# Performance work log

Hardware: AMD Instinct MI355X
Metric: run time of the kernel (lower is better)

## Reference

```python
import jax, jax.numpy as jnp
import numpy as np

RETURN_INDEX = 0  # return_index init kwarg
D_MODEL = 64
NUM_FEATURES = 362


def setup_inputs() -> dict:
    key = jax.random.key(0)
    k1, k2, k3, k4, k5 = jax.random.split(key, 5)
    B, S, N, F, D = 4, 128, 512, NUM_FEATURES, D_MODEL
    x = jax.random.normal(k1, (B, S, N, F), dtype=jnp.float32)
    s = 1.0 / np.sqrt(F)  # torch nn.Linear default init bound
    Wg_w = jax.random.uniform(k2, (D, F), minval=-s, maxval=s, dtype=jnp.float32)
    Wg_b = jax.random.uniform(k3, (D,), minval=-s, maxval=s, dtype=jnp.float32)
    Wh_w = jax.random.uniform(k4, (D, F), minval=-s, maxval=s, dtype=jnp.float32)
    Wh_b = jax.random.uniform(k5, (D,), minval=-s, maxval=s, dtype=jnp.float32)
    return {"x": x, "Wg_w": Wg_w, "Wg_b": Wg_b, "Wh_w": Wh_w, "Wh_b": Wh_b}


def reference(x, Wg_w, Wg_b, Wh_w, Wh_b):
    # x: [B, S, N, F]. Haar dwt -> idwt(cA,None)/idwt(None,cD) collapses to:
    #   rec_l[2k] = rec_l[2k+1] = (x[2k]+x[2k+1])/2
    #   rec_h[2k] = -rec_h[2k+1] = (x[2k]-x[2k+1])/2
    B, S, N, F = x.shape
    r = x[:, :, :, RETURN_INDEX]                      # [B, S, N]
    rp = r.reshape(B, S // 2, 2, N)                   # pair adjacent time steps
    avg = (rp[:, :, 0] + rp[:, :, 1]) * 0.5           # [B, S//2, N]
    diff = (rp[:, :, 0] - rp[:, :, 1]) * 0.5          # [B, S//2, N]
    X_l = jnp.stack([avg, avg], axis=2).reshape(B, S, N)
    X_h = jnp.stack([diff, -diff], axis=2).reshape(B, S, N)
    X_l_full = x.at[:, :, :, RETURN_INDEX].set(X_l)
    X_h_full = x.at[:, :, :, RETURN_INDEX].set(X_h)
    X_l_proj = jnp.einsum('bsnf,df->bsnd', X_l_full, Wg_w) + Wg_b
    X_h_proj = jnp.einsum('bsnf,df->bsnd', X_h_full, Wh_w) + Wh_b
    return (X_l_proj, X_h_proj)
```

## Files before the change

kernel.cpp:

```cpp
#include <hip/hip_runtime.h>
#include <hip/hip_bf16.h>
#include <stdint.h>

#define M_ROWS (4*128*512)
#define FDIM 362
#define TROWS 16
#define ROWB 1448
#define TILEB (TROWS*ROWB)
#define CPW 362
#define GRID 1024
#define TPB 16
#define OUT_HALF 16777216

typedef __attribute__((ext_vector_type(8))) short bf16x8;
typedef __attribute__((ext_vector_type(4))) float f32x4;

template<int N> struct Ic { static constexpr int value = N; };

__device__ __forceinline__ bf16x8 pack8(float2 a, float2 b, float2 c, float2 d) {
  union { __hip_bfloat162 h[4]; bf16x8 v; } t;
  t.h[0] = __float22bfloat162_rn(a);
  t.h[1] = __float22bfloat162_rn(b);
  t.h[2] = __float22bfloat162_rn(c);
  t.h[3] = __float22bfloat162_rn(d);
  return t.v;
}
__device__ __forceinline__ float2 ld2(const float* p) { return *(const float2*)p; }

__global__ __launch_bounds__(256, 2) void dfl_kernel(
    const float* __restrict__ x,
    const float* __restrict__ Wg,
    const float* __restrict__ Wgb,
    const float* __restrict__ Wh,
    const float* __restrict__ Whb,
    float* __restrict__ out)
{
  __shared__ __attribute__((aligned(16))) unsigned char Ab[3][TILEB];
  __shared__ __attribute__((aligned(16))) unsigned char tb[4*2048];

  const int tid  = threadIdx.x;
  const int lane = tid & 63;
  const int wv   = tid >> 6;
  const int q    = lane >> 4;
  const int l15  = lane & 15;
  const bool is_h = wv >= 2;
  const int colb  = (wv & 1) * 32;
  const float* Wsel  = is_h ? Wh  : Wg;
  const float* Wbsel = is_h ? Whb : Wgb;

  bf16x8 bw[2][12];
  float biasf[2], w0f[2];
#pragma unroll
  for (int f = 0; f < 2; ++f) {
    const int dloc = colb + f*16 + l15;
    const float* wrow = Wsel + (size_t)dloc * FDIM;
    biasf[f] = Wbsel[dloc];
    w0f[f]   = wrow[0];
#pragma unroll
    for (int k = 0; k < 12; ++k) {
      float2 t0 = make_float2(0.f,0.f), t1 = t0, t2 = t0, t3 = t0;
      if (k < 11) {
        const float* p = wrow + k*32 + q*8;
        t0 = ld2(p); t1 = ld2(p+2); t2 = ld2(p+4); t3 = ld2(p+6);
      } else if (q == 0) {
        t0 = ld2(wrow+352); t1 = ld2(wrow+354); t2 = ld2(wrow+356); t3 = ld2(wrow+358);
      } else if (q == 1) {
        t0 = ld2(wrow+360);
      }
      bw[f][k] = pack8(t0, t1, t2, t3);
    }
  }

  auto stage = [&](int tile, int p) {
    const unsigned char* src = (const unsigned char*)(x + (size_t)tile * TROWS * FDIM);
    unsigned char* dst = &Ab[p][0];
#pragma unroll
    for (int j = 0; j < 6; ++j) {
      const int cbase = wv*CPW + j*64;
      if (lane < CPW - j*64) {
        __builtin_amdgcn_global_load_lds(
            (const __attribute__((address_space(1))) unsigned int*)(src + (size_t)(cbase + lane)*16),
            (__attribute__((address_space(3))) unsigned int*)(dst + cbase*16),
            16, 0, 0);
      }
    }
  };

  unsigned char* wb = tb + wv*2048;
  float* outp = out + (is_h ? OUT_HALF : 0) + colb;

  auto round = [&](int i, auto sflag, auto wc) {
    const int p  = i % 3;
    const int m0 = ((int)blockIdx.x + i*GRID) * TROWS;

    const float rp = x[(size_t)((m0 ^ 512) + l15) * FDIM];
    __builtin_amdgcn_sched_barrier(0);
    if constexpr (decltype(sflag)::value)
      stage((int)blockIdx.x + (i+2)*GRID, (i+2) % 3);
    __builtin_amdgcn_sched_barrier(0);

    const unsigned char* AbP = &Ab[p][0];
    const unsigned char* ap  = AbP + l15*ROWB + q*32;
    f32x4 acc0 = {biasf[0],biasf[0],biasf[0],biasf[0]};
    f32x4 acc1 = {biasf[1],biasf[1],biasf[1],biasf[1]};
#pragma unroll
    for (int k = 0; k < 11; ++k) {
      const unsigned char* pk = ap + k*128;
      bf16x8 av = pack8(*(const float2*)pk, *(const float2*)(pk+8),
                        *(const float2*)(pk+16), *(const float2*)(pk+24));
      acc0 = __builtin_amdgcn_mfma_f32_16x16x32_bf16(av, bw[0][k], acc0, 0,0,0);
      acc1 = __builtin_amdgcn_mfma_f32_16x16x32_bf16(av, bw[1][k], acc1, 0,0,0);
    }
    {
      const unsigned char* pk = ap + 11*128;
      float2 z2 = make_float2(0.f,0.f), f0 = z2, f1 = z2, f2 = z2, f3 = z2;
      if (q == 0) {
        f0 = *(const float2*)pk;      f1 = *(const float2*)(pk+8);
        f2 = *(const float2*)(pk+16); f3 = *(const float2*)(pk+24);
      } else if (q == 1) {
        f0 = *(const float2*)pk;
      }
      bf16x8 av = pack8(f0, f1, f2, f3);
      acc0 = __builtin_amdgcn_mfma_f32_16x16x32_bf16(av, bw[0][11], acc0, 0,0,0);
      acc1 = __builtin_amdgcn_mfma_f32_16x16x32_bf16(av, bw[1][11], acc1, 0,0,0);
    }

    const float rs = *(const float*)(AbP + l15*ROWB);
    const float cval = is_h ? -(rs + rp)*0.5f : (rp - rs)*0.5f;

#pragma unroll
    for (int jj = 0; jj < 4; ++jj) {
      const float cc = __shfl(cval, q*4 + jj, 64);
      const int rl = q*4 + jj;
#pragma unroll
      for (int fn = 0; fn < 2; ++fn) {
        const float v = (fn ? acc1[jj] : acc0[jj]) + cc * w0f[fn];
        const int col = fn*16 + l15;
        const int boff = rl*128 + ((((col>>2) ^ (rl&7))) << 4) + ((col&3) << 2);
        *(float*)(wb + boff) = v;
      }
    }
#pragma unroll
    for (int s = 0; s < 2; ++s) {
      const int rr = s*8 + (lane >> 3);
      const int cs = lane & 7;
      f32x4 vv = *(const f32x4*)(wb + rr*128 + (((cs ^ (rr&7))) << 4));
      *(f32x4*)(outp + (size_t)(m0 + rr)*64 + cs*4) = vv;
    }

    __builtin_amdgcn_sched_barrier(0);
    if constexpr (decltype(wc)::value >= 0) {
      asm volatile("s_waitcnt vmcnt(%0)" :: "i"(decltype(wc)::value) : "memory");
      __builtin_amdgcn_s_barrier();
    }
    __builtin_amdgcn_sched_barrier(0);
  };

  __builtin_amdgcn_sched_barrier(0);
  asm volatile("s_waitcnt vmcnt(0)" ::: "memory");
  stage((int)blockIdx.x, 0);
  stage((int)blockIdx.x + GRID, 1);
  __builtin_amdgcn_sched_barrier(0);
  asm volatile("s_waitcnt vmcnt(6)" ::: "memory");
  __builtin_amdgcn_s_barrier();
  __builtin_amdgcn_sched_barrier(0);

  round(0, Ic<1>{}, Ic<9>{});
  for (int i = 1; i <= 13; ++i) round(i, Ic<1>{}, Ic<11>{});
  round(14, Ic<0>{}, Ic<5>{});
  round(15, Ic<0>{}, Ic<-1>{});
}

extern "C" void kernel_launch(void* const* d_in, const int* in_sizes, int n_in,
                              void* d_out, int out_size, void* d_ws, size_t ws_size,
                              hipStream_t stream) {
  (void)in_sizes; (void)n_in; (void)d_ws; (void)ws_size; (void)out_size;
  const float* x   = (const float*)d_in[0];
  const float* Wg  = (const float*)d_in[1];
  const float* Wgb = (const float*)d_in[2];
  const float* Wh  = (const float*)d_in[3];
  const float* Whb = (const float*)d_in[4];
  float* out = (float*)d_out;
  dfl_kernel<<<GRID, 256, 0, stream>>>(x, Wg, Wgb, Wh, Whb, out);
}
```

Baseline: 117.2 us.

## Switch to double-buffered LDS staging with three blocks per CU

Replaces the hand-scheduled triple-buffered pipeline (fixed 16 rounds, explicit vmcnt waits) with a double-buffered grid-stride loop using __syncthreads. It shrinks the LDS footprint (two tile buffers, a halved transpose buffer written in two halves) and raises launch bounds to 3 blocks per CU with a 768-block grid. The aim is more resident waves to hide memory latency. The trade-off is a shallower prefetch and coarser full waits at each barrier. With 2048 tiles over 768 blocks, work is uneven across blocks.

```diff
diff --git a/kernel.cpp b/kernel.cpp
--- a/kernel.cpp
+++ b/kernel.cpp
@@ -8,14 +8,14 @@
 #define ROWB 1448
 #define TILEB (TROWS*ROWB)
 #define CPW 362
-#define GRID 1024
-#define TPB 16
+#define NTILES (M_ROWS/TROWS)
+#define GRID 768
 #define OUT_HALF 16777216
 
 typedef __attribute__((ext_vector_type(8))) short bf16x8;
 typedef __attribute__((ext_vector_type(4))) float f32x4;
 
-template<int N> struct Ic { static constexpr int value = N; };
+__device__ __forceinline__ float2 ld2(const float* p) { return *(const float2*)p; }
 
 __device__ __forceinline__ bf16x8 pack8(float2 a, float2 b, float2 c, float2 d) {
   union { __hip_bfloat162 h[4]; bf16x8 v; } t;
@@ -25,9 +25,8 @@
   t.h[3] = __float22bfloat162_rn(d);
   return t.v;
 }
-__device__ __forceinline__ float2 ld2(const float* p) { return *(const float2*)p; }
 
-__global__ __launch_bounds__(256, 2) void dfl_kernel(
+__global__ __launch_bounds__(256, 3) void dfl_kernel(
     const float* __restrict__ x,
     const float* __restrict__ Wg,
     const float* __restrict__ Wgb,
@@ -35,8 +34,8 @@
     const float* __restrict__ Whb,
     float* __restrict__ out)
 {
-  __shared__ __attribute__((aligned(16))) unsigned char Ab[3][TILEB];
-  __shared__ __attribute__((aligned(16))) unsigned char tb[4*2048];
+  __shared__ __attribute__((aligned(16))) unsigned char Ab[2][TILEB];
+  __shared__ __attribute__((aligned(16))) unsigned char tb[4*1024];
 
   const int tid  = threadIdx.x;
   const int lane = tid & 63;
@@ -86,21 +85,24 @@
     }
   };
 
-  unsigned char* wb = tb + wv*2048;
+  unsigned char* wb = tb + wv*1024;
   float* outp = out + (is_h ? OUT_HALF : 0) + colb;
 
-  auto round = [&](int i, auto sflag, auto wc) {
-    const int p  = i % 3;
-    const int m0 = ((int)blockIdx.x + i*GRID) * TROWS;
+  int t = (int)blockIdx.x;
+  stage(t, 0);
+  __syncthreads();
+
+  for (int i = 0; t < NTILES; t += GRID, ++i) {
+    const int p  = i & 1;
+    const int m0 = t * TROWS;
+    const int tn = t + GRID;
+    if (tn < NTILES) stage(tn, p ^ 1);
 
     const float rp = x[(size_t)((m0 ^ 512) + l15) * FDIM];
-    __builtin_amdgcn_sched_barrier(0);
-    if constexpr (decltype(sflag)::value)
-      stage((int)blockIdx.x + (i+2)*GRID, (i+2) % 3);
-    __builtin_amdgcn_sched_barrier(0);
 
     const unsigned char* AbP = &Ab[p][0];
     const unsigned char* ap  = AbP + l15*ROWB + q*32;
+
     f32x4 acc0 = {biasf[0],biasf[0],biasf[0],biasf[0]};
     f32x4 acc1 = {biasf[1],biasf[1],biasf[1],biasf[1]};
 #pragma unroll
@@ -129,46 +131,30 @@
     const float cval = is_h ? -(rs + rp)*0.5f : (rp - rs)*0.5f;
 
 #pragma unroll
-    for (int jj = 0; jj < 4; ++jj) {
-      const float cc = __shfl(cval, q*4 + jj, 64);
-      const int rl = q*4 + jj;
+    for (int half = 0; half < 2; ++half) {
 #pragma unroll
-      for (int fn = 0; fn < 2; ++fn) {
-        const float v = (fn ? acc1[jj] : acc0[jj]) + cc * w0f[fn];
-        const int col = fn*16 + l15;
-        const int boff = rl*128 + ((((col>>2) ^ (rl&7))) << 4) + ((col&3) << 2);
-        *(float*)(wb + boff) = v;
+      for (int jj = 0; jj < 4; ++jj) {
+        const int rl = q*4 + jj;
+        const float cc = __shfl(cval, rl, 64);
+        if ((rl >> 3) == half) {
+          const int r7 = rl & 7;
+#pragma unroll
+          for (int fn = 0; fn < 2; ++fn) {
+            const float v = (fn ? acc1[jj] : acc0[jj]) + cc * w0f[fn];
+            const int col = fn*16 + l15;
+            const int boff = r7*128 + ((((col>>2) ^ r7)) << 4) + ((col&3) << 2);
+            *(float*)(wb + boff) = v;
+          }
+        }
       }
-    }
-#pragma unroll
-    for (int s = 0; s < 2; ++s) {
-      const int rr = s*8 + (lane >> 3);
+      const int rr = half*8 + (lane >> 3);
       const int cs = lane & 7;
-      f32x4 vv = *(const f32x4*)(wb + rr*128 + (((cs ^ (rr&7))) << 4));
+      f32x4 vv = *(const f32x4*)(wb + (rr&7)*128 + (((cs ^ (rr&7))) << 4));
       *(f32x4*)(outp + (size_t)(m0 + rr)*64 + cs*4) = vv;
     }
 
-    __builtin_amdgcn_sched_barrier(0);
-    if constexpr (decltype(wc)::value >= 0) {
-      asm volatile("s_waitcnt vmcnt(%0)" :: "i"(decltype(wc)::value) : "memory");
-      __builtin_amdgcn_s_barrier();
-    }
-    __builtin_amdgcn_sched_barrier(0);
-  };
-
-  __builtin_amdgcn_sched_barrier(0);
-  asm volatile("s_waitcnt vmcnt(0)" ::: "memory");
-  stage((int)blockIdx.x, 0);
-  stage((int)blockIdx.x + GRID, 1);
-  __builtin_amdgcn_sched_barrier(0);
-  asm volatile("s_waitcnt vmcnt(6)" ::: "memory");
-  __builtin_amdgcn_s_barrier();
-  __builtin_amdgcn_sched_barrier(0);
-
-  round(0, Ic<1>{}, Ic<9>{});
-  for (int i = 1; i <= 13; ++i) round(i, Ic<1>{}, Ic<11>{});
-  round(14, Ic<0>{}, Ic<5>{});
-  round(15, Ic<0>{}, Ic<-1>{});
+    __syncthreads();
+  }
 }
 
 extern "C" void kernel_launch(void* const* d_in, const int* in_sizes, int n_in,
```

Result: slower. 149.8 us (+27.8%).

## Use persistent blocks with contiguous tiles and a six-deep LDS prefetch ring

Applied to the files above, without the earlier changes.

The grid drops from 1024 to 256 blocks. Each block now processes 64 consecutive 16-row tiles instead of 16 tiles spread across the grid. The shared-memory ring grows from 3 to 6 tile buffers, with five tiles prefetched ahead, and the vmcnt wait thresholds are retuned to match. The aim is more bytes in flight per CU and contiguous DRAM access to better hide global-load latency, at the cost of roughly one resident block per CU because the larger LDS footprint cuts occupancy.

```diff
diff --git a/kernel.cpp b/kernel.cpp
--- a/kernel.cpp
+++ b/kernel.cpp
@@ -8,14 +8,17 @@
 #define ROWB 1448
 #define TILEB (TROWS*ROWB)
 #define CPW 362
-#define GRID 1024
-#define TPB 16
+#define NBUF 6
+#define GRID 256
+#define ROUNDS 64
 #define OUT_HALF 16777216
 
 typedef __attribute__((ext_vector_type(8))) short bf16x8;
 typedef __attribute__((ext_vector_type(4))) float f32x4;
 
 template<int N> struct Ic { static constexpr int value = N; };
+
+__device__ __forceinline__ float2 ld2(const float* p) { return *(const float2*)p; }
 
 __device__ __forceinline__ bf16x8 pack8(float2 a, float2 b, float2 c, float2 d) {
   union { __hip_bfloat162 h[4]; bf16x8 v; } t;
@@ -25,7 +28,6 @@
   t.h[3] = __float22bfloat162_rn(d);
   return t.v;
 }
-__device__ __forceinline__ float2 ld2(const float* p) { return *(const float2*)p; }
 
 __global__ __launch_bounds__(256, 2) void dfl_kernel(
     const float* __restrict__ x,
@@ -35,7 +37,7 @@
     const float* __restrict__ Whb,
     float* __restrict__ out)
 {
-  __shared__ __attribute__((aligned(16))) unsigned char Ab[3][TILEB];
+  __shared__ __attribute__((aligned(16))) unsigned char Ab[NBUF][TILEB];
   __shared__ __attribute__((aligned(16))) unsigned char tb[4*2048];
 
   const int tid  = threadIdx.x;
@@ -47,6 +49,7 @@
   const int colb  = (wv & 1) * 32;
   const float* Wsel  = is_h ? Wh  : Wg;
   const float* Wbsel = is_h ? Whb : Wgb;
+  const int t0 = (int)blockIdx.x * ROUNDS;
 
   bf16x8 bw[2][12];
   float biasf[2], w0f[2];
@@ -58,22 +61,22 @@
     w0f[f]   = wrow[0];
 #pragma unroll
     for (int k = 0; k < 12; ++k) {
-      float2 t0 = make_float2(0.f,0.f), t1 = t0, t2 = t0, t3 = t0;
+      float2 u0 = make_float2(0.f,0.f), u1 = u0, u2 = u0, u3 = u0;
       if (k < 11) {
         const float* p = wrow + k*32 + q*8;
-        t0 = ld2(p); t1 = ld2(p+2); t2 = ld2(p+4); t3 = ld2(p+6);
+        u0 = ld2(p); u1 = ld2(p+2); u2 = ld2(p+4); u3 = ld2(p+6);
       } else if (q == 0) {
-        t0 = ld2(wrow+352); t1 = ld2(wrow+354); t2 = ld2(wrow+356); t3 = ld2(wrow+358);
+        u0 = ld2(wrow+352); u1 = ld2(wrow+354); u2 = ld2(wrow+356); u3 = ld2(wrow+358);
       } else if (q == 1) {
-        t0 = ld2(wrow+360);
+        u0 = ld2(wrow+360);
       }
-      bw[f][k] = pack8(t0, t1, t2, t3);
+      bw[f][k] = pack8(u0, u1, u2, u3);
     }
   }
 
-  auto stage = [&](int tile, int p) {
+  auto stage = [&](int tile, int ps) {
     const unsigned char* src = (const unsigned char*)(x + (size_t)tile * TROWS * FDIM);
-    unsigned char* dst = &Ab[p][0];
+    unsigned char* dst = &Ab[0][0] + ps*TILEB;
 #pragma unroll
     for (int j = 0; j < 6; ++j) {
       const int cbase = wv*CPW + j*64;
@@ -89,17 +92,16 @@
   unsigned char* wb = tb + wv*2048;
   float* outp = out + (is_h ? OUT_HALF : 0) + colb;
 
-  auto round = [&](int i, auto sflag, auto wc) {
-    const int p  = i % 3;
-    const int m0 = ((int)blockIdx.x + i*GRID) * TROWS;
+  auto round = [&](int i, int pcur, int pstage, auto sflag, auto wc) {
+    const int m0 = (t0 + i) * TROWS;
 
     const float rp = x[(size_t)((m0 ^ 512) + l15) * FDIM];
     __builtin_amdgcn_sched_barrier(0);
     if constexpr (decltype(sflag)::value)
-      stage((int)blockIdx.x + (i+2)*GRID, (i+2) % 3);
+      stage(t0 + i + 5, pstage);
     __builtin_amdgcn_sched_barrier(0);
 
-    const unsigned char* AbP = &Ab[p][0];
+    const unsigned char* AbP = &Ab[0][0] + pcur*TILEB;
     const unsigned char* ap  = AbP + l15*ROWB + q*32;
     f32x4 acc0 = {biasf[0],biasf[0],biasf[0],biasf[0]};
     f32x4 acc1 = {biasf[1],biasf[1],biasf[1],biasf[1]};
@@ -158,17 +160,29 @@
 
   __builtin_amdgcn_sched_barrier(0);
   asm volatile("s_waitcnt vmcnt(0)" ::: "memory");
-  stage((int)blockIdx.x, 0);
-  stage((int)blockIdx.x + GRID, 1);
+  stage(t0+0, 0); stage(t0+1, 1); stage(t0+2, 2); stage(t0+3, 3); stage(t0+4, 4);
   __builtin_amdgcn_sched_barrier(0);
-  asm volatile("s_waitcnt vmcnt(6)" ::: "memory");
+  asm volatile("s_waitcnt vmcnt(24)" ::: "memory");
   __builtin_amdgcn_s_barrier();
   __builtin_amdgcn_sched_barrier(0);
 
-  round(0, Ic<1>{}, Ic<9>{});
-  for (int i = 1; i <= 13; ++i) round(i, Ic<1>{}, Ic<11>{});
-  round(14, Ic<0>{}, Ic<5>{});
-  round(15, Ic<0>{}, Ic<-1>{});
+  round(0, 0, 5, Ic<1>{}, Ic<27>{});
+  round(1, 1, 0, Ic<1>{}, Ic<30>{});
+  round(2, 2, 1, Ic<1>{}, Ic<33>{});
+  round(3, 3, 2, Ic<1>{}, Ic<36>{});
+  {
+    int pc = 4, ps = 3;
+    for (int i = 4; i <= 58; ++i) {
+      round(i, pc, ps, Ic<1>{}, Ic<38>{});
+      pc = (pc == 5) ? 0 : pc + 1;
+      ps = (ps == 5) ? 0 : ps + 1;
+    }
+  }
+  round(59, 5, 0, Ic<0>{}, Ic<32>{});
+  round(60, 0, 0, Ic<0>{}, Ic<26>{});
+  round(61, 1, 0, Ic<0>{}, Ic<20>{});
+  round(62, 2, 0, Ic<0>{}, Ic<14>{});
+  round(63, 3, 0, Ic<0>{}, Ic<-1>{});
 }
 
 extern "C" void kernel_launch(void* const* d_in, const int* in_sizes, int n_in,
```

After: 151.0 us. 1.29x slower.
